# Performance work log

Hardware: AMD Instinct MI355X
Metric: run time of the kernel (lower is better)

The kernel has to match this reference:

```python
import jax, jax.numpy as jnp
import numpy as np

A = 0.7071067811865476  # sqrt(2)/2
B_ = 1.0 - A
KH = KW = 3
K2 = 9
STRIDE = 1
PAD = 1
DIL = 1


def setup_inputs() -> dict:
    key = jax.random.key(0)
    k1, k2, k3, k4 = jax.random.split(key, 4)
    Bn, Cin, H, W = 4, 256, 64, 64
    Cout = 256
    x = jax.random.normal(k1, (Bn, Cin, H, W), dtype=jnp.float32)
    offset = jax.random.normal(k2, (Bn, 2 * K2, H, W), dtype=jnp.float32)
    mask = jax.random.uniform(k3, (Bn, K2, H, W), dtype=jnp.float32)
    stdv = 1.0 / np.sqrt(Cin * KH * KW)
    weight = jax.random.uniform(k4, (Cout, Cin, KH, KW), dtype=jnp.float32,
                                minval=-stdv, maxval=stdv)
    bias = jnp.zeros((Cout,), dtype=jnp.float32)
    return {"input": x, "offset": offset, "mask": mask, "weight": weight, "bias": bias}


def _weight_circle(weight):
    # Blend 3x3 corner taps along the diagonal "circle", as in DCNv2_Circle.forward.
    O, C = weight.shape[0], weight.shape[1]
    w = weight.reshape(O, C, K2)
    w0 = A * (A * w[:, :, 0] + B_ * w[:, :, 1]) + B_ * (A * w[:, :, 3] + B_ * w[:, :, 4])
    w2 = A * (B_ * w[:, :, 1] + A * w[:, :, 2]) + B_ * (B_ * w[:, :, 4] + A * w[:, :, 5])
    w6 = B_ * (A * w[:, :, 3] + B_ * w[:, :, 4]) + A * (A * w[:, :, 6] + B_ * w[:, :, 7])
    w8 = B_ * (B_ * w[:, :, 4] + A * w[:, :, 5]) + A * (B_ * w[:, :, 7] + A * w[:, :, 8])
    return jnp.stack([w0, w[:, :, 1], w2, w[:, :, 3], w[:, :, 4],
                      w[:, :, 5], w6, w[:, :, 7], w8], axis=-1)  # [O, C, 9]


def _dcn_v2(x, offset, mask, w_flat, bias):
    Bn, C, H, W = x.shape
    Ho = (H + 2 * PAD - DIL * (KH - 1) - 1) // STRIDE + 1
    Wo = (W + 2 * PAD - DIL * (KW - 1) - 1) // STRIDE + 1
    # Base sampling grid per kernel tap k: [K2, Ho, Wo]
    ki, kj = jnp.meshgrid(jnp.arange(KH), jnp.arange(KW), indexing="ij")
    ki = ki.reshape(K2).astype(jnp.float32)
    kj = kj.reshape(K2).astype(jnp.float32)
    oy = (jnp.arange(Ho, dtype=jnp.float32) * STRIDE - PAD)
    ox = (jnp.arange(Wo, dtype=jnp.float32) * STRIDE - PAD)
    base_y = oy[None, :, None] + DIL * ki[:, None, None]  # [K2, Ho, 1]
    base_x = ox[None, None, :] + DIL * kj[:, None, None]  # [K2, 1, Wo]
    # Offsets: channel 2k is dy, 2k+1 is dx (DCNv2 layout).
    off = offset.reshape(Bn, K2, 2, Ho, Wo)
    y = base_y[None] + off[:, :, 0]  # [B, K2, Ho, Wo]
    x_ = base_x[None] + off[:, :, 1]
    y0 = jnp.floor(y)
    x0 = jnp.floor(x_)
    ly = y - y0
    lx = x_ - x0
    y0i = y0.astype(jnp.int32)
    x0i = x0.astype(jnp.int32)
    flat = x.reshape(Bn, C, H * W)

    def gather(yi, xi):
        valid = (yi >= 0) & (yi < H) & (xi >= 0) & (xi < W)
        idx = jnp.clip(yi, 0, H - 1) * W + jnp.clip(xi, 0, W - 1)  # [B,K2,Ho,Wo]
        v = jax.vmap(lambda f, i: f[:, i.reshape(-1)])(flat, idx)  # [B,C,K2*Ho*Wo]
        v = v.reshape(Bn, C, K2, Ho, Wo)
        return v * valid[:, None].astype(v.dtype)

    hy = 1.0 - ly
    hx = 1.0 - lx
    # corner weights broadcast over channel dim
    sampled = (gather(y0i, x0i) * (hy * hx)[:, None]
               + gather(y0i, x0i + 1) * (hy * lx)[:, None]
               + gather(y0i + 1, x0i) * (ly * hx)[:, None]
               + gather(y0i + 1, x0i + 1) * (ly * lx)[:, None])  # [B,C,K2,Ho,Wo]
    sampled = sampled * mask[:, None]  # modulation
    out = jnp.einsum("bckhw,ock->bohw", sampled, w_flat)
    return out + bias[None, :, None, None]


def reference(input, offset, mask, weight, bias):
    w_flat = _weight_circle(weight)
    return _dcn_v2(input, offset, mask, w_flat, bias)
```

## Files before the change

### kernel.cpp

```cpp
#include <hip/hip_runtime.h>

typedef __bf16 bf16x8 __attribute__((ext_vector_type(8)));
typedef float f32x4 __attribute__((ext_vector_type(4)));

#define HH 64
#define WW 64
#define HW 4096
#define COUT 256
#define BSTRIDE 296
#define NROWS 12
#define XROW 65
#define XS_OFF 37888

__device__ __forceinline__ void bar_sync() {
    asm volatile("s_waitcnt lgkmcnt(0)" ::: "memory");
    __builtin_amdgcn_s_barrier();
    asm volatile("" ::: "memory");
}

__global__ __launch_bounds__(256) void prep_weights(const float* __restrict__ weight,
                                                    __bf16* __restrict__ wp) {
    const int t = blockIdx.x * 256 + threadIdx.x;
    const int lane = t & 63;
    const int tm   = (t >> 6) & 15;
    const int cg   = (t >> 10) & 7;
    const int tap  = t >> 13;
    const int rr = lane & 15, q = lane >> 4;
    const int o  = tm * 16 + rr;
    const int c0 = cg * 32 + q * 8;
    const float* wb = weight + ((size_t)o * 256 + c0) * 9;
    const float Af = 0.70710678118654752f;
    const float Bf = 1.0f - Af;
    bf16x8 v;
    #pragma unroll
    for (int j = 0; j < 8; ++j) {
        const float* w = wb + j * 9;
        float r;
        switch (tap) {
            case 0:  r = Af*(Af*w[0]+Bf*w[1]) + Bf*(Af*w[3]+Bf*w[4]); break;
            case 1:  r = w[1]; break;
            case 2:  r = Af*(Bf*w[1]+Af*w[2]) + Bf*(Bf*w[4]+Af*w[5]); break;
            case 3:  r = w[3]; break;
            case 4:  r = w[4]; break;
            case 5:  r = w[5]; break;
            case 6:  r = Bf*(Af*w[3]+Bf*w[4]) + Af*(Af*w[6]+Bf*w[7]); break;
            case 7:  r = w[7]; break;
            default: r = Bf*(Bf*w[4]+Af*w[5]) + Af*(Bf*w[7]+Af*w[8]); break;
        }
        v[j] = (__bf16)r;
    }
    const int ksg = cg * 9 + tap;
    *(bf16x8*)&wp[(size_t)(((ksg * 16 + tm) << 6) | lane) << 3] = v;
}

__global__ __launch_bounds__(512, 2) void dcn_main(
        const float* __restrict__ x, const float* __restrict__ off,
        const float* __restrict__ msk, const __bf16* __restrict__ wp,
        const float* __restrict__ bias, float* __restrict__ out) {
    __shared__ char smem[65536];
    __bf16* Xs = (__bf16*)(smem + XS_OFF);
    char* BsB  = smem;
    const char* XsB = (const char*)smem + XS_OFF;

    const int tid  = threadIdx.x;
    const int wv   = tid >> 6;
    const int lane = tid & 63;
    const int q    = lane >> 4, rr = lane & 15;
    const int px   = lane;

    const int bid = blockIdx.x;
    const int xcd = bid & 7;
    const int b   = xcd >> 1;
    const int h   = ((xcd & 1) << 5) | (bid >> 3);

    const int rowbase = min(max(h - 5, 0), HH - NROWS);
    const float* xb = x + (size_t)b * 256 * HW;

    int SGk[3], GOFF[3], XA[3];
    #pragma unroll
    for (int k = 0; k < 3; ++k) {
        int slot = k * 512 + tid;
        int sg   = slot / 768;
        int rem  = slot - sg * 768;
        int row  = rem >> 6, spx = rem & 63;
        SGk[k]  = sg;
        GOFF[k] = (rowbase + row) * 64 + spx;
        XA[k]   = ((sg * NROWS + row) * XROW + spx) << 3;
    }

    float W00[3], W01[3], W10[3], W11[3];
    int AY0[3], AY1[3], DXO[3], COLB[3], GP[3];
    bool UV[3];
    #pragma unroll
    for (int k = 0; k < 3; ++k) {
        int c = (k < 2) ? (wv + 8 * k) : ((wv >= 6) ? wv + 10 : -1);
        UV[k] = (c >= 0);
        if (UV[k]) {
            int sg = c / 9, tap = c % 9;
            int ki = tap / 3, kj = tap - 3 * ki;
            const float* offp = off + (size_t)b * 18 * HW + h * 64 + px;
            float dy = offp[(2 * tap) * HW];
            float dx = offp[(2 * tap + 1) * HW];
            float mv = msk[(size_t)b * 9 * HW + (size_t)tap * HW + h * 64 + px];
            float py  = (float)(h - 1 + ki) + dy;
            float pxf = (float)(px - 1 + kj) + dx;
            float y0f = floorf(py), x0f = floorf(pxf);
            float ly = py - y0f, lx = pxf - x0f;
            float hy = 1.0f - ly, hx = 1.0f - lx;
            int y0 = (int)y0f, x0 = (int)x0f;
            int y1 = y0 + 1, x1 = x0 + 1;
            bool vy0 = (y0 >= 0) && (y0 < HH), vy1 = (y1 >= 0) && (y1 < HH);
            bool vx0 = (x0 >= 0) && (x0 < WW), vx1 = (x1 >= 0) && (x1 < WW);
            int cy0 = min(max(y0, 0), HH - 1), cy1 = min(max(y1, 0), HH - 1);
            int cx0 = min(max(x0, 0), WW - 1), cx1 = min(max(x1, 0), WW - 1);
            W00[k] = (vy0 && vx0) ? hy * hx * mv : 0.0f;
            W01[k] = (vy0 && vx1) ? hy * lx * mv : 0.0f;
            W10[k] = (vy1 && vx0) ? ly * hx * mv : 0.0f;
            W11[k] = (vy1 && vx1) ? ly * lx * mv : 0.0f;
            int ry0 = min(max(cy0 - rowbase, 0), NROWS - 1);
            int ry1 = min(max(cy1 - rowbase, 0), NROWS - 1);
            bool useG = (vy0 && (cy0 < rowbase || cy0 > rowbase + NROWS - 1))
                     || (vy1 && (cy1 < rowbase || cy1 > rowbase + NROWS - 1));
            AY0[k]  = ((sg * NROWS + ry0) * XROW + cx0) * 16;
            AY1[k]  = ((sg * NROWS + ry1) * XROW + cx0) * 16;
            DXO[k]  = (cx1 - cx0) * 16;
            COLB[k] = (tap * 32 + sg * 8) * 2;
            GP[k]   = cy0 | (cy1 << 6) | (cx0 << 12) | (cx1 << 18) | (sg << 24)
                    | (useG ? (1u << 31) : 0);
        }
    }

    f32x4 acc[4][4];
    #pragma unroll
    for (int i = 0; i < 4; ++i)
        #pragma unroll
        for (int n = 0; n < 4; ++n)
            acc[i][n] = (f32x4)0.0f;

    const int tm0   = (wv & 3) * 4;
    const int klbeg = (wv & 4) ? 5 : 0;
    const int nkl   = (wv & 4) ? 4 : 5;

    float R[3][8];
    #pragma unroll
    for (int k = 0; k < 3; ++k) {
        const float* p = xb + (size_t)(SGk[k] * 8) * HW + GOFF[k];
        #pragma unroll
        for (int j = 0; j < 8; ++j) R[k][j] = p[j * HW];
    }

    #pragma unroll 1
    for (int s = 0; s < 16; ++s) {
        const int cg = s >> 1, half = s & 1;
        bar_sync();
        #pragma unroll
        for (int k = 0; k < 3; ++k) {
            bf16x8 v;
            #pragma unroll
            for (int j = 0; j < 8; ++j) v[j] = (__bf16)R[k][j];
            *(bf16x8*)&Xs[XA[k]] = v;
        }
        if (s < 15) {
            const int s1 = s + 1;
            const int cbase = (s1 >> 1) * 32 + (s1 & 1) * 16;
            #pragma unroll
            for (int k = 0; k < 3; ++k) {
                const float* p = xb + (size_t)(cbase + SGk[k] * 8) * HW + GOFF[k];
                #pragma unroll
                for (int j = 0; j < 8; ++j) R[k][j] = p[j * HW];
            }
        }
        bar_sync();
        #pragma unroll
        for (int k = 0; k < 3; ++k) {
            if (UV[k]) {
                bf16x8 c00 = *(const bf16x8*)(XsB + AY0[k]);
                bf16x8 c01 = *(const bf16x8*)(XsB + AY0[k] + DXO[k]);
                bf16x8 c10 = *(const bf16x8*)(XsB + AY1[k]);
                bf16x8 c11 = *(const bf16x8*)(XsB + AY1[k] + DXO[k]);
                float w0 = W00[k], w1 = W01[k], w2 = W10[k], w3 = W11[k];
                bf16x8 res;
                #pragma unroll
                for (int j = 0; j < 8; ++j) {
                    float v = w0 * (float)c00[j] + w1 * (float)c01[j]
                            + w2 * (float)c10[j] + w3 * (float)c11[j];
                    res[j] = (__bf16)v;
                }
                int gp = GP[k];
                if (gp < 0) {
                    int cy0 = gp & 63, cy1 = (gp >> 6) & 63;
                    int cx0 = (gp >> 12) & 63, cx1 = (gp >> 18) & 63;
                    int sg = (gp >> 24) & 3;
                    const float* xc = xb + (size_t)(cg * 32 + half * 16 + sg * 8) * HW;
                    int i00 = cy0 * 64 + cx0, i01 = cy0 * 64 + cx1;
                    int i10 = cy1 * 64 + cx0, i11 = cy1 * 64 + cx1;
                    #pragma unroll
                    for (int j = 0; j < 8; ++j) {
                        float v = w0 * xc[i00] + w1 * xc[i01]
                                + w2 * xc[i10] + w3 * xc[i11];
                        res[j] = (__bf16)v;
                        xc += HW;
                    }
                }
                *(bf16x8*)(BsB + px * 592 + COLB[k] + half * 32) = res;
            }
        }
        if (half) {
            bar_sync();
            const __bf16* ap = wp + ((size_t)((cg * 9 + klbeg) * 16 + tm0) * 64 + lane) * 8;
            bf16x8 a0 = *(const bf16x8*)ap;
            bf16x8 a1 = *(const bf16x8*)(ap + 512);
            bf16x8 a2 = *(const bf16x8*)(ap + 1024);
            bf16x8 a3 = *(const bf16x8*)(ap + 1536);
            int kc = (klbeg * 32 + q * 8) * 2;
            #pragma unroll 1
            for (int t = 0; t < nkl; ++t) {
                bf16x8 n0 = a0, n1 = a1, n2 = a2, n3 = a3;
                if (t + 1 < nkl) {
                    const __bf16* np = ap + 8192;
                    n0 = *(const bf16x8*)np;
                    n1 = *(const bf16x8*)(np + 512);
                    n2 = *(const bf16x8*)(np + 1024);
                    n3 = *(const bf16x8*)(np + 1536);
                }
                const char* bp = BsB + rr * 592 + kc;
                bf16x8 bb0 = *(const bf16x8*)(bp);
                bf16x8 bb1 = *(const bf16x8*)(bp + 16 * 592);
                bf16x8 bb2 = *(const bf16x8*)(bp + 32 * 592);
                bf16x8 bb3 = *(const bf16x8*)(bp + 48 * 592);
                acc[0][0] = __builtin_amdgcn_mfma_f32_16x16x32_bf16(a0, bb0, acc[0][0], 0, 0, 0);
                acc[1][0] = __builtin_amdgcn_mfma_f32_16x16x32_bf16(a1, bb0, acc[1][0], 0, 0, 0);
                acc[2][0] = __builtin_amdgcn_mfma_f32_16x16x32_bf16(a2, bb0, acc[2][0], 0, 0, 0);
                acc[3][0] = __builtin_amdgcn_mfma_f32_16x16x32_bf16(a3, bb0, acc[3][0], 0, 0, 0);
                acc[0][1] = __builtin_amdgcn_mfma_f32_16x16x32_bf16(a0, bb1, acc[0][1], 0, 0, 0);
                acc[1][1] = __builtin_amdgcn_mfma_f32_16x16x32_bf16(a1, bb1, acc[1][1], 0, 0, 0);
                acc[2][1] = __builtin_amdgcn_mfma_f32_16x16x32_bf16(a2, bb1, acc[2][1], 0, 0, 0);
                acc[3][1] = __builtin_amdgcn_mfma_f32_16x16x32_bf16(a3, bb1, acc[3][1], 0, 0, 0);
                acc[0][2] = __builtin_amdgcn_mfma_f32_16x16x32_bf16(a0, bb2, acc[0][2], 0, 0, 0);
                acc[1][2] = __builtin_amdgcn_mfma_f32_16x16x32_bf16(a1, bb2, acc[1][2], 0, 0, 0);
                acc[2][2] = __builtin_amdgcn_mfma_f32_16x16x32_bf16(a2, bb2, acc[2][2], 0, 0, 0);
                acc[3][2] = __builtin_amdgcn_mfma_f32_16x16x32_bf16(a3, bb2, acc[3][2], 0, 0, 0);
                acc[0][3] = __builtin_amdgcn_mfma_f32_16x16x32_bf16(a0, bb3, acc[0][3], 0, 0, 0);
                acc[1][3] = __builtin_amdgcn_mfma_f32_16x16x32_bf16(a1, bb3, acc[1][3], 0, 0, 0);
                acc[2][3] = __builtin_amdgcn_mfma_f32_16x16x32_bf16(a2, bb3, acc[2][3], 0, 0, 0);
                acc[3][3] = __builtin_amdgcn_mfma_f32_16x16x32_bf16(a3, bb3, acc[3][3], 0, 0, 0);
                ap += 8192;
                kc += 64;
                a0 = n0; a1 = n1; a2 = n2; a3 = n3;
            }
        }
    }

    float* scr = (float*)smem;
    bar_sync();
    if (wv >= 4) {
        const int base = (wv - 4) * 4096 + lane * 4;
        #pragma unroll
        for (int i = 0; i < 4; ++i)
            #pragma unroll
            for (int n = 0; n < 4; ++n)
                *(f32x4*)&scr[base + (i * 4 + n) * 256] = acc[i][n];
    }
    bar_sync();
    if (wv < 4) {
        const int mrow = wv * 64;
        const int base = wv * 4096 + lane * 4;
        #pragma unroll
        for (int i = 0; i < 4; ++i) {
            #pragma unroll
            for (int n = 0; n < 4; ++n) {
                f32x4 p = *(const f32x4*)&scr[base + (i * 4 + n) * 256];
                #pragma unroll
                for (int e = 0; e < 4; ++e) {
                    int m = mrow + i * 16 + q * 4 + e;
                    out[((size_t)b * COUT + m) * HW + h * 64 + n * 16 + rr]
                        = acc[i][n][e] + p[e] + bias[m];
                }
            }
        }
    }
}

extern "C" void kernel_launch(void* const* d_in, const int* in_sizes, int n_in,
                              void* d_out, int out_size, void* d_ws, size_t ws_size,
                              hipStream_t stream) {
    const float* x      = (const float*)d_in[0];
    const float* off    = (const float*)d_in[1];
    const float* msk    = (const float*)d_in[2];
    const float* weight = (const float*)d_in[3];
    const float* bias   = (const float*)d_in[4];
    float* out = (float*)d_out;

    __bf16* wp = (__bf16*)d_ws;

    prep_weights<<<288, 256, 0, stream>>>(weight, wp);
    dcn_main<<<256, 512, 0, stream>>>(x, off, msk, wp, bias, out);
}
```

Measured before the change: 123.7 us.

## Pipeline sampling and MFMA with ring-buffered swizzled B tile and double-buffered X

```diff
diff --git a/kernel.cpp b/kernel.cpp
--- a/kernel.cpp
+++ b/kernel.cpp
@@ -7,10 +7,10 @@
 #define WW 64
 #define HW 4096
 #define COUT 256
-#define BSTRIDE 296
 #define NROWS 12
 #define XROW 65
-#define XS_OFF 37888
+#define XS_OFF 32768
+#define XSBUF 12480
 
 __device__ __forceinline__ void bar_sync() {
     asm volatile("s_waitcnt lgkmcnt(0)" ::: "memory");
@@ -20,15 +20,14 @@
 
 __global__ __launch_bounds__(256) void prep_weights(const float* __restrict__ weight,
                                                     __bf16* __restrict__ wp) {
-    const int t = blockIdx.x * 256 + threadIdx.x;
-    const int lane = t & 63;
-    const int tm   = (t >> 6) & 15;
-    const int cg   = (t >> 10) & 7;
-    const int tap  = t >> 13;
-    const int rr = lane & 15, q = lane >> 4;
-    const int o  = tm * 16 + rr;
-    const int c0 = cg * 32 + q * 8;
-    const float* wb = weight + ((size_t)o * 256 + c0) * 9;
+    const int kb  = blockIdx.x;
+    const int tid = threadIdx.x;
+    const int tap = kb % 9;
+    const int g   = kb / 9;
+    const int rr  = tid & 15;
+    const int tm  = tid >> 4;
+    const int o   = tm * 16 + rr;
+    const float* wb = weight + ((size_t)o * 256 + g * 8) * 9;
     const float Af = 0.70710678118654752f;
     const float Bf = 1.0f - Af;
     bf16x8 v;
@@ -49,8 +48,7 @@
         }
         v[j] = (__bf16)r;
     }
-    const int ksg = cg * 9 + tap;
-    *(bf16x8*)&wp[(size_t)(((ksg * 16 + tm) << 6) | lane) << 3] = v;
+    *(bf16x8*)&wp[((size_t)kb * 256 + tid) * 8] = v;
 }
 
 __global__ __launch_bounds__(512, 2) void dcn_main(
@@ -58,9 +56,6 @@
         const float* __restrict__ msk, const __bf16* __restrict__ wp,
         const float* __restrict__ bias, float* __restrict__ out) {
     __shared__ char smem[65536];
-    __bf16* Xs = (__bf16*)(smem + XS_OFF);
-    char* BsB  = smem;
-    const char* XsB = (const char*)smem + XS_OFF;
 
     const int tid  = threadIdx.x;
     const int wv   = tid >> 6;
@@ -68,6 +63,9 @@
     const int q    = lane >> 4, rr = lane & 15;
     const int px   = lane;
 
+    const int mg  = wv & 3;
+    const int klp = wv >> 2;
+
     const int bid = blockIdx.x;
     const int xcd = bid & 7;
     const int b   = xcd >> 1;
@@ -76,27 +74,19 @@
     const int rowbase = min(max(h - 5, 0), HH - NROWS);
     const float* xb = x + (size_t)b * 256 * HW;
 
-    int SGk[3], GOFF[3], XA[3];
+    const int GOFF_A = (rowbase + wv) * 64 + lane;
+    const int GOFF_B = (rowbase + 8 + wv) * 64 + lane;
+    const int XA_A   = (wv * XROW + lane) * 16;
+    const int XA_B   = ((8 + wv) * XROW + lane) * 16;
+    const bool hasB  = (wv < 4);
+
+    float W00[2], W01[2], W10[2], W11[2];
+    int AY0[2], AY1[2], DXO[2], TAP8[2], GP[2];
+    const bool UV1 = (wv == 0);
     #pragma unroll
-    for (int k = 0; k < 3; ++k) {
-        int slot = k * 512 + tid;
-        int sg   = slot / 768;
-        int rem  = slot - sg * 768;
-        int row  = rem >> 6, spx = rem & 63;
-        SGk[k]  = sg;
-        GOFF[k] = (rowbase + row) * 64 + spx;
-        XA[k]   = ((sg * NROWS + row) * XROW + spx) << 3;
-    }
-
-    float W00[3], W01[3], W10[3], W11[3];
-    int AY0[3], AY1[3], DXO[3], COLB[3], GP[3];
-    bool UV[3];
-    #pragma unroll
-    for (int k = 0; k < 3; ++k) {
-        int c = (k < 2) ? (wv + 8 * k) : ((wv >= 6) ? wv + 10 : -1);
-        UV[k] = (c >= 0);
-        if (UV[k]) {
-            int sg = c / 9, tap = c % 9;
+    for (int k = 0; k < 2; ++k) {
+        if (k == 0 || UV1) {
+            int tap = (k == 0) ? wv : 8;
             int ki = tap / 3, kj = tap - 3 * ki;
             const float* offp = off + (size_t)b * 18 * HW + h * 64 + px;
             float dy = offp[(2 * tap) * HW];
@@ -121,11 +111,11 @@
             int ry1 = min(max(cy1 - rowbase, 0), NROWS - 1);
             bool useG = (vy0 && (cy0 < rowbase || cy0 > rowbase + NROWS - 1))
                      || (vy1 && (cy1 < rowbase || cy1 > rowbase + NROWS - 1));
-            AY0[k]  = ((sg * NROWS + ry0) * XROW + cx0) * 16;
-            AY1[k]  = ((sg * NROWS + ry1) * XROW + cx0) * 16;
+            AY0[k]  = (ry0 * XROW + cx0) * 16;
+            AY1[k]  = (ry1 * XROW + cx0) * 16;
             DXO[k]  = (cx1 - cx0) * 16;
-            COLB[k] = (tap * 32 + sg * 8) * 2;
-            GP[k]   = cy0 | (cy1 << 6) | (cx0 << 12) | (cx1 << 18) | (sg << 24)
+            TAP8[k] = tap * 8;
+            GP[k]   = cy0 | (cy1 << 6) | (cx0 << 12) | (cx1 << 18)
                     | (useG ? (1u << 31) : 0);
         }
     }
@@ -137,117 +127,129 @@
         for (int n = 0; n < 4; ++n)
             acc[i][n] = (f32x4)0.0f;
 
-    const int tm0   = (wv & 3) * 4;
-    const int klbeg = (wv & 4) ? 5 : 0;
-    const int nkl   = (wv & 4) ? 4 : 5;
-
-    float R[3][8];
-    #pragma unroll
-    for (int k = 0; k < 3; ++k) {
-        const float* p = xb + (size_t)(SGk[k] * 8) * HW + GOFF[k];
+    float R[2][8];
+    {
+        const float* pA = xb + GOFF_A;
         #pragma unroll
-        for (int j = 0; j < 8; ++j) R[k][j] = p[j * HW];
-    }
+        for (int j = 0; j < 8; ++j) R[0][j] = pA[j * HW];
+        if (hasB) {
+            const float* pB = xb + GOFF_B;
+            #pragma unroll
+            for (int j = 0; j < 8; ++j) R[1][j] = pB[j * HW];
+        }
+    }
+
+    const char* wpB = (const char*)wp;
+    const char* ap = wpB + (size_t)(4 * klp + q) * 4096 + mg * 1024 + rr * 16;
+    bf16x8 a0 = *(const bf16x8*)ap;
+    bf16x8 a1 = *(const bf16x8*)(ap + 256);
+    bf16x8 a2 = *(const bf16x8*)(ap + 512);
+    bf16x8 a3 = *(const bf16x8*)(ap + 768);
+    int kwp = klp;
+
+    const int sw8 = (lane & 7) << 3;
 
     #pragma unroll 1
-    for (int s = 0; s < 16; ++s) {
-        const int cg = s >> 1, half = s & 1;
+    for (int s = 0; s <= 33; ++s) {
         bar_sync();
-        #pragma unroll
-        for (int k = 0; k < 3; ++k) {
-            bf16x8 v;
-            #pragma unroll
-            for (int j = 0; j < 8; ++j) v[j] = (__bf16)R[k][j];
-            *(bf16x8*)&Xs[XA[k]] = v;
-        }
-        if (s < 15) {
-            const int s1 = s + 1;
-            const int cbase = (s1 >> 1) * 32 + (s1 & 1) * 16;
-            #pragma unroll
-            for (int k = 0; k < 3; ++k) {
-                const float* p = xb + (size_t)(cbase + SGk[k] * 8) * HW + GOFF[k];
+        if (s < 32) {
+            char* xw = smem + XS_OFF + (s & 1) * XSBUF;
+            bf16x8 vA;
+            #pragma unroll
+            for (int j = 0; j < 8; ++j) vA[j] = (__bf16)R[0][j];
+            *(bf16x8*)(xw + XA_A) = vA;
+            if (hasB) {
+                bf16x8 vB;
                 #pragma unroll
-                for (int j = 0; j < 8; ++j) R[k][j] = p[j * HW];
-            }
-        }
-        bar_sync();
-        #pragma unroll
-        for (int k = 0; k < 3; ++k) {
-            if (UV[k]) {
-                bf16x8 c00 = *(const bf16x8*)(XsB + AY0[k]);
-                bf16x8 c01 = *(const bf16x8*)(XsB + AY0[k] + DXO[k]);
-                bf16x8 c10 = *(const bf16x8*)(XsB + AY1[k]);
-                bf16x8 c11 = *(const bf16x8*)(XsB + AY1[k] + DXO[k]);
-                float w0 = W00[k], w1 = W01[k], w2 = W10[k], w3 = W11[k];
-                bf16x8 res;
+                for (int j = 0; j < 8; ++j) vB[j] = (__bf16)R[1][j];
+                *(bf16x8*)(xw + XA_B) = vB;
+            }
+        }
+        if (s < 31) {
+            const float* pA = xb + (size_t)((s + 1) * 8) * HW + GOFF_A;
+            #pragma unroll
+            for (int j = 0; j < 8; ++j) R[0][j] = pA[j * HW];
+            if (hasB) {
+                const float* pB = xb + (size_t)((s + 1) * 8) * HW + GOFF_B;
                 #pragma unroll
-                for (int j = 0; j < 8; ++j) {
-                    float v = w0 * (float)c00[j] + w1 * (float)c01[j]
-                            + w2 * (float)c10[j] + w3 * (float)c11[j];
-                    res[j] = (__bf16)v;
-                }
-                int gp = GP[k];
-                if (gp < 0) {
-                    int cy0 = gp & 63, cy1 = (gp >> 6) & 63;
-                    int cx0 = (gp >> 12) & 63, cx1 = (gp >> 18) & 63;
-                    int sg = (gp >> 24) & 3;
-                    const float* xc = xb + (size_t)(cg * 32 + half * 16 + sg * 8) * HW;
-                    int i00 = cy0 * 64 + cx0, i01 = cy0 * 64 + cx1;
-                    int i10 = cy1 * 64 + cx0, i11 = cy1 * 64 + cx1;
+                for (int j = 0; j < 8; ++j) R[1][j] = pB[j * HW];
+            }
+        }
+        if (s >= 1 && s <= 32) {
+            const int g = s - 1;
+            const char* xr = smem + XS_OFF + (g & 1) * XSBUF;
+            const int gb8 = (g * 72) & 255;
+            #pragma unroll
+            for (int k = 0; k < 2; ++k) {
+                if (k == 0 || UV1) {
+                    bf16x8 c00 = *(const bf16x8*)(xr + AY0[k]);
+                    bf16x8 c01 = *(const bf16x8*)(xr + AY0[k] + DXO[k]);
+                    bf16x8 c10 = *(const bf16x8*)(xr + AY1[k]);
+                    bf16x8 c11 = *(const bf16x8*)(xr + AY1[k] + DXO[k]);
+                    float w0 = W00[k], w1 = W01[k], w2 = W10[k], w3 = W11[k];
+                    bf16x8 res;
                     #pragma unroll
                     for (int j = 0; j < 8; ++j) {
-                        float v = w0 * xc[i00] + w1 * xc[i01]
-                                + w2 * xc[i10] + w3 * xc[i11];
+                        float v = w0 * (float)c00[j] + w1 * (float)c01[j]
+                                + w2 * (float)c10[j] + w3 * (float)c11[j];
                         res[j] = (__bf16)v;
-                        xc += HW;
                     }
+                    int gp = GP[k];
+                    if (gp < 0) {
+                        int cy0 = gp & 63, cy1 = (gp >> 6) & 63;
+                        int cx0 = (gp >> 12) & 63, cx1 = (gp >> 18) & 63;
+                        const float* xc = xb + (size_t)(g * 8) * HW;
+                        int i00 = cy0 * 64 + cx0, i01 = cy0 * 64 + cx1;
+                        int i10 = cy1 * 64 + cx0, i11 = cy1 * 64 + cx1;
+                        #pragma unroll
+                        for (int j = 0; j < 8; ++j) {
+                            float v = w0 * xc[i00] + w1 * xc[i01]
+                                    + w2 * xc[i10] + w3 * xc[i11];
+                            res[j] = (__bf16)v;
+                            xc += HW;
+                        }
+                    }
+                    const int colp = ((gb8 + TAP8[k]) & 255) ^ sw8;
+                    *(bf16x8*)(smem + lane * 512 + colp * 2) = res;
                 }
-                *(bf16x8*)(BsB + px * 592 + COLB[k] + half * 32) = res;
-            }
-        }
-        if (half) {
-            bar_sync();
-            const __bf16* ap = wp + ((size_t)((cg * 9 + klbeg) * 16 + tm0) * 64 + lane) * 8;
-            bf16x8 a0 = *(const bf16x8*)ap;
-            bf16x8 a1 = *(const bf16x8*)(ap + 512);
-            bf16x8 a2 = *(const bf16x8*)(ap + 1024);
-            bf16x8 a3 = *(const bf16x8*)(ap + 1536);
-            int kc = (klbeg * 32 + q * 8) * 2;
-            #pragma unroll 1
-            for (int t = 0; t < nkl; ++t) {
-                bf16x8 n0 = a0, n1 = a1, n2 = a2, n3 = a3;
-                if (t + 1 < nkl) {
-                    const __bf16* np = ap + 8192;
-                    n0 = *(const bf16x8*)np;
-                    n1 = *(const bf16x8*)(np + 512);
-                    n2 = *(const bf16x8*)(np + 1024);
-                    n3 = *(const bf16x8*)(np + 1536);
-                }
-                const char* bp = BsB + rr * 592 + kc;
-                bf16x8 bb0 = *(const bf16x8*)(bp);
-                bf16x8 bb1 = *(const bf16x8*)(bp + 16 * 592);
-                bf16x8 bb2 = *(const bf16x8*)(bp + 32 * 592);
-                bf16x8 bb3 = *(const bf16x8*)(bp + 48 * 592);
-                acc[0][0] = __builtin_amdgcn_mfma_f32_16x16x32_bf16(a0, bb0, acc[0][0], 0, 0, 0);
-                acc[1][0] = __builtin_amdgcn_mfma_f32_16x16x32_bf16(a1, bb0, acc[1][0], 0, 0, 0);
-                acc[2][0] = __builtin_amdgcn_mfma_f32_16x16x32_bf16(a2, bb0, acc[2][0], 0, 0, 0);
-                acc[3][0] = __builtin_amdgcn_mfma_f32_16x16x32_bf16(a3, bb0, acc[3][0], 0, 0, 0);
-                acc[0][1] = __builtin_amdgcn_mfma_f32_16x16x32_bf16(a0, bb1, acc[0][1], 0, 0, 0);
-                acc[1][1] = __builtin_amdgcn_mfma_f32_16x16x32_bf16(a1, bb1, acc[1][1], 0, 0, 0);
-                acc[2][1] = __builtin_amdgcn_mfma_f32_16x16x32_bf16(a2, bb1, acc[2][1], 0, 0, 0);
-                acc[3][1] = __builtin_amdgcn_mfma_f32_16x16x32_bf16(a3, bb1, acc[3][1], 0, 0, 0);
-                acc[0][2] = __builtin_amdgcn_mfma_f32_16x16x32_bf16(a0, bb2, acc[0][2], 0, 0, 0);
-                acc[1][2] = __builtin_amdgcn_mfma_f32_16x16x32_bf16(a1, bb2, acc[1][2], 0, 0, 0);
-                acc[2][2] = __builtin_amdgcn_mfma_f32_16x16x32_bf16(a2, bb2, acc[2][2], 0, 0, 0);
-                acc[3][2] = __builtin_amdgcn_mfma_f32_16x16x32_bf16(a3, bb2, acc[3][2], 0, 0, 0);
-                acc[0][3] = __builtin_amdgcn_mfma_f32_16x16x32_bf16(a0, bb3, acc[0][3], 0, 0, 0);
-                acc[1][3] = __builtin_amdgcn_mfma_f32_16x16x32_bf16(a1, bb3, acc[1][3], 0, 0, 0);
-                acc[2][3] = __builtin_amdgcn_mfma_f32_16x16x32_bf16(a2, bb3, acc[2][3], 0, 0, 0);
-                acc[3][3] = __builtin_amdgcn_mfma_f32_16x16x32_bf16(a3, bb3, acc[3][3], 0, 0, 0);
-                ap += 8192;
-                kc += 64;
-                a0 = n0; a1 = n1; a2 = n2; a3 = n3;
-            }
+            }
+        }
+        int k1 = (s >= 2) ? ((72 * (s - 1)) >> 5) : 0;
+        if (k1 > 72) k1 = 72;
+        while (kwp < k1) {
+            bf16x8 n0 = a0, n1 = a1, n2 = a2, n3 = a3;
+            if (kwp + 2 < 72) {
+                const char* np = ap + 32768;
+                n0 = *(const bf16x8*)np;
+                n1 = *(const bf16x8*)(np + 256);
+                n2 = *(const bf16x8*)(np + 512);
+                n3 = *(const bf16x8*)(np + 768);
+            }
+            const int col2 = ((((kwp << 5) + (q << 3)) & 255) ^ ((rr & 7) << 3)) * 2;
+            const char* bp = smem + rr * 512 + col2;
+            bf16x8 bb0 = *(const bf16x8*)(bp);
+            bf16x8 bb1 = *(const bf16x8*)(bp + 16 * 512);
+            bf16x8 bb2 = *(const bf16x8*)(bp + 32 * 512);
+            bf16x8 bb3 = *(const bf16x8*)(bp + 48 * 512);
+            acc[0][0] = __builtin_amdgcn_mfma_f32_16x16x32_bf16(a0, bb0, acc[0][0], 0, 0, 0);
+            acc[1][0] = __builtin_amdgcn_mfma_f32_16x16x32_bf16(a1, bb0, acc[1][0], 0, 0, 0);
+            acc[2][0] = __builtin_amdgcn_mfma_f32_16x16x32_bf16(a2, bb0, acc[2][0], 0, 0, 0);
+            acc[3][0] = __builtin_amdgcn_mfma_f32_16x16x32_bf16(a3, bb0, acc[3][0], 0, 0, 0);
+            acc[0][1] = __builtin_amdgcn_mfma_f32_16x16x32_bf16(a0, bb1, acc[0][1], 0, 0, 0);
+            acc[1][1] = __builtin_amdgcn_mfma_f32_16x16x32_bf16(a1, bb1, acc[1][1], 0, 0, 0);
+            acc[2][1] = __builtin_amdgcn_mfma_f32_16x16x32_bf16(a2, bb1, acc[2][1], 0, 0, 0);
+            acc[3][1] = __builtin_amdgcn_mfma_f32_16x16x32_bf16(a3, bb1, acc[3][1], 0, 0, 0);
+            acc[0][2] = __builtin_amdgcn_mfma_f32_16x16x32_bf16(a0, bb2, acc[0][2], 0, 0, 0);
+            acc[1][2] = __builtin_amdgcn_mfma_f32_16x16x32_bf16(a1, bb2, acc[1][2], 0, 0, 0);
+            acc[2][2] = __builtin_amdgcn_mfma_f32_16x16x32_bf16(a2, bb2, acc[2][2], 0, 0, 0);
+            acc[3][2] = __builtin_amdgcn_mfma_f32_16x16x32_bf16(a3, bb2, acc[3][2], 0, 0, 0);
+            acc[0][3] = __builtin_amdgcn_mfma_f32_16x16x32_bf16(a0, bb3, acc[0][3], 0, 0, 0);
+            acc[1][3] = __builtin_amdgcn_mfma_f32_16x16x32_bf16(a1, bb3, acc[1][3], 0, 0, 0);
+            acc[2][3] = __builtin_amdgcn_mfma_f32_16x16x32_bf16(a2, bb3, acc[2][3], 0, 0, 0);
+            acc[3][3] = __builtin_amdgcn_mfma_f32_16x16x32_bf16(a3, bb3, acc[3][3], 0, 0, 0);
+            ap += 32768;
+            kwp += 2;
+            a0 = n0; a1 = n1; a2 = n2; a3 = n3;
         }
     }
 
```

After: 132.6 us. 1.07x slower.

## Feed sampled values straight into MFMA registers, drop LDS B-tile staging

Applied to the files above, without the earlier changes.

```diff
diff --git a/kernel.cpp b/kernel.cpp
--- a/kernel.cpp
+++ b/kernel.cpp
@@ -1,16 +1,15 @@
 #include <hip/hip_runtime.h>
 
-typedef __bf16 bf16x8 __attribute__((ext_vector_type(8)));
+typedef _Float16 half8 __attribute__((ext_vector_type(8)));
 typedef float f32x4 __attribute__((ext_vector_type(4)));
 
 #define HH 64
 #define WW 64
 #define HW 4096
 #define COUT 256
-#define BSTRIDE 296
 #define NROWS 12
 #define XROW 65
-#define XS_OFF 37888
+#define SGSTRIDE 12480
 
 __device__ __forceinline__ void bar_sync() {
     asm volatile("s_waitcnt lgkmcnt(0)" ::: "memory");
@@ -19,54 +18,60 @@
 }
 
 __global__ __launch_bounds__(256) void prep_weights(const float* __restrict__ weight,
-                                                    __bf16* __restrict__ wp) {
+                                                    _Float16* __restrict__ wp) {
     const int t = blockIdx.x * 256 + threadIdx.x;
     const int lane = t & 63;
     const int tm   = (t >> 6) & 15;
-    const int cg   = (t >> 10) & 7;
-    const int tap  = t >> 13;
+    const int kl   = t >> 10;
     const int rr = lane & 15, q = lane >> 4;
+    const int o4 = 4 * kl + q;
+    const int g  = o4 / 12;
+    const int tt = o4 - g * 12;
     const int o  = tm * 16 + rr;
-    const int c0 = cg * 32 + q * 8;
-    const float* wb = weight + ((size_t)o * 256 + c0) * 9;
-    const float Af = 0.70710678118654752f;
-    const float Bf = 1.0f - Af;
-    bf16x8 v;
-    #pragma unroll
-    for (int j = 0; j < 8; ++j) {
-        const float* w = wb + j * 9;
-        float r;
-        switch (tap) {
-            case 0:  r = Af*(Af*w[0]+Bf*w[1]) + Bf*(Af*w[3]+Bf*w[4]); break;
-            case 1:  r = w[1]; break;
-            case 2:  r = Af*(Bf*w[1]+Af*w[2]) + Bf*(Bf*w[4]+Af*w[5]); break;
-            case 3:  r = w[3]; break;
-            case 4:  r = w[4]; break;
-            case 5:  r = w[5]; break;
-            case 6:  r = Bf*(Af*w[3]+Bf*w[4]) + Af*(Af*w[6]+Bf*w[7]); break;
-            case 7:  r = w[7]; break;
-            default: r = Bf*(Bf*w[4]+Af*w[5]) + Af*(Bf*w[7]+Af*w[8]); break;
-        }
-        v[j] = (__bf16)r;
-    }
-    const int ksg = cg * 9 + tap;
-    *(bf16x8*)&wp[(size_t)(((ksg * 16 + tm) << 6) | lane) << 3] = v;
+    half8 v;
+    #pragma unroll
+    for (int j = 0; j < 8; ++j) v[j] = (_Float16)0.0f;
+    if (tt < 9) {
+        const float Af = 0.70710678118654752f;
+        const float Bf = 1.0f - Af;
+        const float* wb = weight + ((size_t)o * 256 + g * 8) * 9;
+        #pragma unroll
+        for (int j = 0; j < 8; ++j) {
+            const float* w = wb + j * 9;
+            float r;
+            switch (tt) {
+                case 0:  r = Af*(Af*w[0]+Bf*w[1]) + Bf*(Af*w[3]+Bf*w[4]); break;
+                case 1:  r = w[1]; break;
+                case 2:  r = Af*(Bf*w[1]+Af*w[2]) + Bf*(Bf*w[4]+Af*w[5]); break;
+                case 3:  r = w[3]; break;
+                case 4:  r = w[4]; break;
+                case 5:  r = w[5]; break;
+                case 6:  r = Bf*(Af*w[3]+Bf*w[4]) + Af*(Af*w[6]+Bf*w[7]); break;
+                case 7:  r = w[7]; break;
+                default: r = Bf*(Bf*w[4]+Af*w[5]) + Af*(Bf*w[7]+Af*w[8]); break;
+            }
+            v[j] = (_Float16)r;
+        }
+    }
+    *(half8*)&wp[((size_t)(kl * 16 + tm) * 64 + lane) * 8] = v;
 }
 
 __global__ __launch_bounds__(512, 2) void dcn_main(
         const float* __restrict__ x, const float* __restrict__ off,
-        const float* __restrict__ msk, const __bf16* __restrict__ wp,
+        const float* __restrict__ msk, const _Float16* __restrict__ wp,
         const float* __restrict__ bias, float* __restrict__ out) {
-    __shared__ char smem[65536];
-    __bf16* Xs = (__bf16*)(smem + XS_OFF);
-    char* BsB  = smem;
-    const char* XsB = (const char*)smem + XS_OFF;
+    __shared__ char smem[32768];
+    const char* XsB = (const char*)smem;
+    char* XsW = smem;
 
     const int tid  = threadIdx.x;
     const int wv   = tid >> 6;
     const int lane = tid & 63;
     const int q    = lane >> 4, rr = lane & 15;
-    const int px   = lane;
+
+    const int Q = wv & 3;
+    const int p = wv >> 2;
+    const int px = Q * 16 + rr;
 
     const int bid = blockIdx.x;
     const int xcd = bid & 7;
@@ -75,6 +80,7 @@
 
     const int rowbase = min(max(h - 5, 0), HH - NROWS);
     const float* xb = x + (size_t)b * 256 * HW;
+    const char* wpB = (const char*)wp;
 
     int SGk[3], GOFF[3], XA[3];
     #pragma unroll
@@ -85,18 +91,15 @@
         int row  = rem >> 6, spx = rem & 63;
         SGk[k]  = sg;
         GOFF[k] = (rowbase + row) * 64 + spx;
-        XA[k]   = ((sg * NROWS + row) * XROW + spx) << 3;
-    }
-
-    float W00[3], W01[3], W10[3], W11[3];
-    int AY0[3], AY1[3], DXO[3], COLB[3], GP[3];
-    bool UV[3];
-    #pragma unroll
-    for (int k = 0; k < 3; ++k) {
-        int c = (k < 2) ? (wv + 8 * k) : ((wv >= 6) ? wv + 10 : -1);
-        UV[k] = (c >= 0);
-        if (UV[k]) {
-            int sg = c / 9, tap = c % 9;
+        XA[k]   = ((sg * NROWS + row) * XROW + spx) * 16;
+    }
+
+    _Float16 W00h[3], W01h[3], W10h[3], W11h[3];
+    int AYp[3], GPp[3];
+    #pragma unroll
+    for (int r = 0; r < 3; ++r) {
+        const int tap = 4 * r + q;
+        if (tap < 9) {
             int ki = tap / 3, kj = tap - 3 * ki;
             const float* offp = off + (size_t)b * 18 * HW + h * 64 + px;
             float dy = offp[(2 * tap) * HW];
@@ -113,168 +116,125 @@
             bool vx0 = (x0 >= 0) && (x0 < WW), vx1 = (x1 >= 0) && (x1 < WW);
             int cy0 = min(max(y0, 0), HH - 1), cy1 = min(max(y1, 0), HH - 1);
             int cx0 = min(max(x0, 0), WW - 1), cx1 = min(max(x1, 0), WW - 1);
-            W00[k] = (vy0 && vx0) ? hy * hx * mv : 0.0f;
-            W01[k] = (vy0 && vx1) ? hy * lx * mv : 0.0f;
-            W10[k] = (vy1 && vx0) ? ly * hx * mv : 0.0f;
-            W11[k] = (vy1 && vx1) ? ly * lx * mv : 0.0f;
+            W00h[r] = (_Float16)((vy0 && vx0) ? hy * hx * mv : 0.0f);
+            W01h[r] = (_Float16)((vy0 && vx1) ? hy * lx * mv : 0.0f);
+            W10h[r] = (_Float16)((vy1 && vx0) ? ly * hx * mv : 0.0f);
+            W11h[r] = (_Float16)((vy1 && vx1) ? ly * lx * mv : 0.0f);
             int ry0 = min(max(cy0 - rowbase, 0), NROWS - 1);
             int ry1 = min(max(cy1 - rowbase, 0), NROWS - 1);
             bool useG = (vy0 && (cy0 < rowbase || cy0 > rowbase + NROWS - 1))
                      || (vy1 && (cy1 < rowbase || cy1 > rowbase + NROWS - 1));
-            AY0[k]  = ((sg * NROWS + ry0) * XROW + cx0) * 16;
-            AY1[k]  = ((sg * NROWS + ry1) * XROW + cx0) * 16;
-            DXO[k]  = (cx1 - cx0) * 16;
-            COLB[k] = (tap * 32 + sg * 8) * 2;
-            GP[k]   = cy0 | (cy1 << 6) | (cx0 << 12) | (cx1 << 18) | (sg << 24)
-                    | (useG ? (1u << 31) : 0);
-        }
-    }
-
-    f32x4 acc[4][4];
-    #pragma unroll
-    for (int i = 0; i < 4; ++i)
+            AYp[r] = ((ry0 * XROW + cx0) * 16) | (((ry1 * XROW + cx0) * 16) << 16);
+            GPp[r] = cy0 | (cy1 << 6) | (cx0 << 12) | (cx1 << 18)
+                   | ((cx1 - cx0) << 24) | (useG ? (1u << 31) : 0);
+        } else {
+            W00h[r] = (_Float16)0.0f; W01h[r] = (_Float16)0.0f;
+            W10h[r] = (_Float16)0.0f; W11h[r] = (_Float16)0.0f;
+            AYp[r] = 0; GPp[r] = 0;
+        }
+    }
+
+    f32x4 acc[16];
+    #pragma unroll
+    for (int t = 0; t < 16; ++t) acc[t] = (f32x4)0.0f;
+
+    float R[3][8];
+    #pragma unroll
+    for (int k = 0; k < 3; ++k) {
+        const float* pp = xb + (size_t)(SGk[k] * 8) * HW + GOFF[k];
         #pragma unroll
-        for (int n = 0; n < 4; ++n)
-            acc[i][n] = (f32x4)0.0f;
-
-    const int tm0   = (wv & 3) * 4;
-    const int klbeg = (wv & 4) ? 5 : 0;
-    const int nkl   = (wv & 4) ? 4 : 5;
-
-    float R[3][8];
-    #pragma unroll
-    for (int k = 0; k < 3; ++k) {
-        const float* p = xb + (size_t)(SGk[k] * 8) * HW + GOFF[k];
-        #pragma unroll
-        for (int j = 0; j < 8; ++j) R[k][j] = p[j * HW];
-    }
+        for (int j = 0; j < 8; ++j) R[k][j] = pp[j * HW];
+    }
+
+#define KSTEP(KL, RSEL, SGO, GB) do {                                         \
+    const int ayp_ = AYp[RSEL]; const int gpp_ = GPp[RSEL];                   \
+    const int a0_ = (ayp_ & 0xffff) + (SGO) * SGSTRIDE;                       \
+    const int a1_ = ((int)((unsigned)ayp_ >> 16)) + (SGO) * SGSTRIDE;         \
+    const int dxo_ = (gpp_ & (1 << 24)) ? 16 : 0;                             \
+    half8 c00 = *(const half8*)(XsB + a0_);                                   \
+    half8 c01 = *(const half8*)(XsB + a0_ + dxo_);                            \
+    half8 c10 = *(const half8*)(XsB + a1_);                                   \
+    half8 c11 = *(const half8*)(XsB + a1_ + dxo_);                            \
+    half8 res = c00 * W00h[RSEL] + c01 * W01h[RSEL]                           \
+              + c10 * W10h[RSEL] + c11 * W11h[RSEL];                          \
+    if (gpp_ < 0) {                                                           \
+        int cy0_ = gpp_ & 63, cy1_ = (gpp_ >> 6) & 63;                        \
+        int cx0_ = (gpp_ >> 12) & 63, cx1_ = (gpp_ >> 18) & 63;               \
+        const float* xc_ = xb + (size_t)((GB) * 8) * HW;                      \
+        float w0_ = (float)W00h[RSEL], w1_ = (float)W01h[RSEL];               \
+        float w2_ = (float)W10h[RSEL], w3_ = (float)W11h[RSEL];               \
+        int i00_ = cy0_ * 64 + cx0_, i01_ = cy0_ * 64 + cx1_;                 \
+        int i10_ = cy1_ * 64 + cx0_, i11_ = cy1_ * 64 + cx1_;                 \
+        _Pragma("unroll")                                                     \
+        for (int j = 0; j < 8; ++j) {                                         \
+            float v_ = w0_ * xc_[i00_] + w1_ * xc_[i01_]                      \
+                     + w2_ * xc_[i10_] + w3_ * xc_[i11_];                     \
+            res[j] = (_Float16)v_; xc_ += HW;                                 \
+        }                                                                     \
+    }                                                                         \
+    const char* ap_ = wpB + (size_t)(KL) * 16384 + lane * 16;                 \
+    half8 af[16];                                                             \
+    _Pragma("unroll")                                                         \
+    for (int t = 0; t < 16; ++t) af[t] = *(const half8*)(ap_ + t * 1024);     \
+    _Pragma("unroll")                                                         \
+    for (int t = 0; t < 16; ++t)                                              \
+        acc[t] = __builtin_amdgcn_mfma_f32_16x16x32_f16(af[t], res, acc[t],   \
+                                                        0, 0, 0);             \
+} while (0)
 
     #pragma unroll 1
     for (int s = 0; s < 16; ++s) {
-        const int cg = s >> 1, half = s & 1;
         bar_sync();
         #pragma unroll
         for (int k = 0; k < 3; ++k) {
-            bf16x8 v;
-            #pragma unroll
-            for (int j = 0; j < 8; ++j) v[j] = (__bf16)R[k][j];
-            *(bf16x8*)&Xs[XA[k]] = v;
+            half8 v;
+            #pragma unroll
+            for (int j = 0; j < 8; ++j) v[j] = (_Float16)R[k][j];
+            *(half8*)(XsW + XA[k]) = v;
         }
         if (s < 15) {
-            const int s1 = s + 1;
-            const int cbase = (s1 >> 1) * 32 + (s1 & 1) * 16;
+            const int cbase = (s + 1) * 16;
             #pragma unroll
             for (int k = 0; k < 3; ++k) {
-                const float* p = xb + (size_t)(cbase + SGk[k] * 8) * HW + GOFF[k];
+                const float* pp = xb + (size_t)(cbase + SGk[k] * 8) * HW + GOFF[k];
                 #pragma unroll
-                for (int j = 0; j < 8; ++j) R[k][j] = p[j * HW];
+                for (int j = 0; j < 8; ++j) R[k][j] = pp[j * HW];
             }
         }
         bar_sync();
-        #pragma unroll
-        for (int k = 0; k < 3; ++k) {
-            if (UV[k]) {
-                bf16x8 c00 = *(const bf16x8*)(XsB + AY0[k]);
-                bf16x8 c01 = *(const bf16x8*)(XsB + AY0[k] + DXO[k]);
-                bf16x8 c10 = *(const bf16x8*)(XsB + AY1[k]);
-                bf16x8 c11 = *(const bf16x8*)(XsB + AY1[k] + DXO[k]);
-                float w0 = W00[k], w1 = W01[k], w2 = W10[k], w3 = W11[k];
-                bf16x8 res;
-                #pragma unroll
-                for (int j = 0; j < 8; ++j) {
-                    float v = w0 * (float)c00[j] + w1 * (float)c01[j]
-                            + w2 * (float)c10[j] + w3 * (float)c11[j];
-                    res[j] = (__bf16)v;
-                }
-                int gp = GP[k];
-                if (gp < 0) {
-                    int cy0 = gp & 63, cy1 = (gp >> 6) & 63;
-                    int cx0 = (gp >> 12) & 63, cx1 = (gp >> 18) & 63;
-                    int sg = (gp >> 24) & 3;
-                    const float* xc = xb + (size_t)(cg * 32 + half * 16 + sg * 8) * HW;
-                    int i00 = cy0 * 64 + cx0, i01 = cy0 * 64 + cx1;
-                    int i10 = cy1 * 64 + cx0, i11 = cy1 * 64 + cx1;
-                    #pragma unroll
-                    for (int j = 0; j < 8; ++j) {
-                        float v = w0 * xc[i00] + w1 * xc[i01]
-                                + w2 * xc[i10] + w3 * xc[i11];
-                        res[j] = (__bf16)v;
-                        xc += HW;
-                    }
-                }
-                *(bf16x8*)(BsB + px * 592 + COLB[k] + half * 32) = res;
-            }
-        }
-        if (half) {
-            bar_sync();
-            const __bf16* ap = wp + ((size_t)((cg * 9 + klbeg) * 16 + tm0) * 64 + lane) * 8;
-            bf16x8 a0 = *(const bf16x8*)ap;
-            bf16x8 a1 = *(const bf16x8*)(ap + 512);
-            bf16x8 a2 = *(const bf16x8*)(ap + 1024);
-            bf16x8 a3 = *(const bf16x8*)(ap + 1536);
-            int kc = (klbeg * 32 + q * 8) * 2;
-            #pragma unroll 1
-            for (int t = 0; t < nkl; ++t) {
-                bf16x8 n0 = a0, n1 = a1, n2 = a2, n3 = a3;
-                if (t + 1 < nkl) {
-                    const __bf16* np = ap + 8192;
-                    n0 = *(const bf16x8*)np;
-                    n1 = *(const bf16x8*)(np + 512);
-                    n2 = *(const bf16x8*)(np + 1024);
-                    n3 = *(const bf16x8*)(np + 1536);
-                }
-                const char* bp = BsB + rr * 592 + kc;
-                bf16x8 bb0 = *(const bf16x8*)(bp);
-                bf16x8 bb1 = *(const bf16x8*)(bp + 16 * 592);
-                bf16x8 bb2 = *(const bf16x8*)(bp + 32 * 592);
-                bf16x8 bb3 = *(const bf16x8*)(bp + 48 * 592);
-                acc[0][0] = __builtin_amdgcn_mfma_f32_16x16x32_bf16(a0, bb0, acc[0][0], 0, 0, 0);
-                acc[1][0] = __builtin_amdgcn_mfma_f32_16x16x32_bf16(a1, bb0, acc[1][0], 0, 0, 0);
-                acc[2][0] = __builtin_amdgcn_mfma_f32_16x16x32_bf16(a2, bb0, acc[2][0], 0, 0, 0);
-                acc[3][0] = __builtin_amdgcn_mfma_f32_16x16x32_bf16(a3, bb0, acc[3][0], 0, 0, 0);
-                acc[0][1] = __builtin_amdgcn_mfma_f32_16x16x32_bf16(a0, bb1, acc[0][1], 0, 0, 0);
-                acc[1][1] = __builtin_amdgcn_mfma_f32_16x16x32_bf16(a1, bb1, acc[1][1], 0, 0, 0);
-                acc[2][1] = __builtin_amdgcn_mfma_f32_16x16x32_bf16(a2, bb1, acc[2][1], 0, 0, 0);
-                acc[3][1] = __builtin_amdgcn_mfma_f32_16x16x32_bf16(a3, bb1, acc[3][1], 0, 0, 0);
-                acc[0][2] = __builtin_amdgcn_mfma_f32_16x16x32_bf16(a0, bb2, acc[0][2], 0, 0, 0);
-                acc[1][2] = __builtin_amdgcn_mfma_f32_16x16x32_bf16(a1, bb2, acc[1][2], 0, 0, 0);
-                acc[2][2] = __builtin_amdgcn_mfma_f32_16x16x32_bf16(a2, bb2, acc[2][2], 0, 0, 0);
-                acc[3][2] = __builtin_amdgcn_mfma_f32_16x16x32_bf16(a3, bb2, acc[3][2], 0, 0, 0);
-                acc[0][3] = __builtin_amdgcn_mfma_f32_16x16x32_bf16(a0, bb3, acc[0][3], 0, 0, 0);
-                acc[1][3] = __builtin_amdgcn_mfma_f32_16x16x32_bf16(a1, bb3, acc[1][3], 0, 0, 0);
-                acc[2][3] = __builtin_amdgcn_mfma_f32_16x16x32_bf16(a2, bb3, acc[2][3], 0, 0, 0);
-                acc[3][3] = __builtin_amdgcn_mfma_f32_16x16x32_bf16(a3, bb3, acc[3][3], 0, 0, 0);
-                ap += 8192;
-                kc += 64;
-                a0 = n0; a1 = n1; a2 = n2; a3 = n3;
-            }
-        }
-    }
+        const int kl0 = 6 * s;
+        const int g0 = 2 * s, g1 = 2 * s + 1;
+        if (p == 0) {
+            KSTEP(kl0 + 0, 0, 0, g0);
+            KSTEP(kl0 + 2, 2, 0, g0);
+            KSTEP(kl0 + 4, 1, 1, g1);
+        } else {
+            KSTEP(kl0 + 1, 1, 0, g0);
+            KSTEP(kl0 + 3, 0, 1, g1);
+            KSTEP(kl0 + 5, 2, 1, g1);
+        }
+    }
+#undef KSTEP
 
     float* scr = (float*)smem;
-    bar_sync();
-    if (wv >= 4) {
-        const int base = (wv - 4) * 4096 + lane * 4;
-        #pragma unroll
-        for (int i = 0; i < 4; ++i)
-            #pragma unroll
-            for (int n = 0; n < 4; ++n)
-                *(f32x4*)&scr[base + (i * 4 + n) * 256] = acc[i][n];
-    }
-    bar_sync();
-    if (wv < 4) {
-        const int mrow = wv * 64;
-        const int base = wv * 4096 + lane * 4;
-        #pragma unroll
-        for (int i = 0; i < 4; ++i) {
-            #pragma unroll
-            for (int n = 0; n < 4; ++n) {
-                f32x4 p = *(const f32x4*)&scr[base + (i * 4 + n) * 256];
+    #pragma unroll 1
+    for (int rd = 0; rd < 2; ++rd) {
+        bar_sync();
+        if (p == 1) {
+            #pragma unroll
+            for (int tt = 0; tt < 8; ++tt)
+                *(f32x4*)&scr[((Q * 8 + tt) * 64 + lane) * 4] = acc[rd * 8 + tt];
+        }
+        bar_sync();
+        if (p == 0) {
+            #pragma unroll
+            for (int tt = 0; tt < 8; ++tt) {
+                f32x4 pr = *(const f32x4*)&scr[((Q * 8 + tt) * 64 + lane) * 4];
                 #pragma unroll
                 for (int e = 0; e < 4; ++e) {
-                    int m = mrow + i * 16 + q * 4 + e;
-                    out[((size_t)b * COUT + m) * HW + h * 64 + n * 16 + rr]
-                        = acc[i][n][e] + p[e] + bias[m];
+                    int m = (rd * 8 + tt) * 16 + q * 4 + e;
+                    out[((size_t)b * COUT + m) * HW + h * 64 + px]
+                        = acc[rd * 8 + tt][e] + pr[e] + bias[m];
                 }
             }
         }
@@ -291,8 +251,8 @@
     const float* bias   = (const float*)d_in[4];
     float* out = (float*)d_out;
 
-    __bf16* wp = (__bf16*)d_ws;
-
-    prep_weights<<<288, 256, 0, stream>>>(weight, wp);
+    _Float16* wp = (_Float16*)d_ws;
+
+    prep_weights<<<384, 256, 0, stream>>>(weight, wp);
     dcn_main<<<256, 512, 0, stream>>>(x, off, msk, wp, bias, out);
 }
```

New measurement: 315.5 us. 155% more time.
